# Optimization experiments

Measured on AMD Instinct MI355X. Metric: run time of the kernel, lower is better.

Reference implementation:

```python
import math
import jax, jax.numpy as jnp
import numpy as np

H = 16
D_MODEL = 1024
D_K = D_MODEL // H


def setup_inputs() -> dict:
    key = jax.random.key(0)
    ks = jax.random.split(key, 12)
    B, S = 4, 2048
    scale = 1.0 / math.sqrt(D_MODEL)
    inp = {
        "query": jax.random.normal(ks[0], (B, S, D_MODEL), jnp.float32),
        "key": jax.random.normal(ks[1], (B, S, D_MODEL), jnp.float32),
        "value": jax.random.normal(ks[2], (B, S, D_MODEL), jnp.float32),
        "mask": jnp.ones((B, 1, 1, S), jnp.int32),
        "Wq": jax.random.normal(ks[3], (D_MODEL, D_MODEL), jnp.float32) * scale,
        "bq": jnp.zeros((D_MODEL,), jnp.float32),
        "Wk": jax.random.normal(ks[4], (D_MODEL, D_MODEL), jnp.float32) * scale,
        "bk": jnp.zeros((D_MODEL,), jnp.float32),
        "Wv": jax.random.normal(ks[5], (D_MODEL, D_MODEL), jnp.float32) * scale,
        "bv": jnp.zeros((D_MODEL,), jnp.float32),
        "Wo": jax.random.normal(ks[6], (D_MODEL, D_MODEL), jnp.float32) * scale,
        "bo": jnp.zeros((D_MODEL,), jnp.float32),
    }
    return inp


def _split_heads(x, W, b):
    # x: (B, S, d_model) -> (B, H, S, d_k); torch Linear: x @ W.T + b
    B, S, _ = x.shape
    y = x @ W.T + b
    return y.reshape(B, S, H, D_K).transpose(0, 2, 1, 3)


def reference(query, key, value, mask, Wq, bq, Wk, bk, Wv, bv, Wo, bo):
    B, Sq, _ = query.shape
    q = _split_heads(query, Wq, bq)   # (B,H,Sq,dk)
    k = _split_heads(key, Wk, bk)     # (B,H,Skv,dk)
    v = _split_heads(value, Wv, bv)   # (B,H,Skv,dk)
    scores = jnp.einsum('bhqd,bhkd->bhqk', q, k) / math.sqrt(D_K)
    scores = jnp.where(mask == 0, jnp.float32(-1e9), scores)
    p_attn = jax.nn.softmax(scores, axis=-1)  # dropout p=0 (eval)
    x = jnp.einsum('bhqk,bhkd->bhqd', p_attn, v)
    x = x.transpose(0, 2, 1, 3).reshape(B, Sq, H * D_K)
    return x @ Wo.T + bo
```

## Files before the change

kernel.cpp:

```cpp
#include <hip/hip_runtime.h>
#include <hip/hip_bf16.h>
#include <stdint.h>

typedef unsigned short u16;
typedef short bf16x8 __attribute__((ext_vector_type(8)));
typedef float f32x4 __attribute__((ext_vector_type(4)));

#define D_MODEL 1024
#define NHEAD 16
#define DK 64
#define SEQ 2048
#define NB 4
#define MTOT (NB * SEQ)

__device__ __forceinline__ u16 f2bf(float f) {
  union { float f; unsigned u; } x; x.f = f;
  unsigned r = x.u + 0x7FFFu + ((x.u >> 16) & 1u);
  return (u16)(r >> 16);
}
#if __has_builtin(__builtin_amdgcn_cvt_pk_bf16_f32)
__device__ __forceinline__ unsigned pkbf(float a, float b) {
  auto r = __builtin_amdgcn_cvt_pk_bf16_f32(a, b);
  union { decltype(r) v; unsigned u; } c; c.v = r; return c.u;
}
#else
__device__ __forceinline__ unsigned pkbf(float a, float b) {
  return (unsigned)f2bf(a) | ((unsigned)f2bf(b) << 16);
}
#endif
__device__ __forceinline__ void gl_lds16(const u16* g, u16* s) {
  __builtin_amdgcn_global_load_lds(
      (const __attribute__((address_space(1))) void*)g,
      (__attribute__((address_space(3))) void*)s, 16, 0, 0);
}

__global__ __launch_bounds__(256) void cvt1(const float4* __restrict__ src,
                                            uint2* __restrict__ dst, int n4) {
  for (int i = blockIdx.x * 256 + threadIdx.x; i < n4; i += gridDim.x * 256) {
    float4 x = src[i];
    uint2 o;
    o.x = pkbf(x.x, x.y);
    o.y = pkbf(x.z, x.w);
    dst[i] = o;
  }
}
__global__ __launch_bounds__(256) void cvt4(const float4* __restrict__ s0,
                                            const float4* __restrict__ s1,
                                            const float4* __restrict__ s2,
                                            const float4* __restrict__ s3,
                                            uint2* __restrict__ dst, int n4each) {
  const float4* s = (blockIdx.y == 0) ? s0 : (blockIdx.y == 1) ? s1
                  : (blockIdx.y == 2) ? s2 : s3;
  uint2* d = dst + (size_t)blockIdx.y * n4each;
  for (int i = blockIdx.x * 256 + threadIdx.x; i < n4each; i += gridDim.x * 256) {
    float4 x = s[i];
    uint2 o;
    o.x = pkbf(x.x, x.y);
    o.y = pkbf(x.z, x.w);
    d[i] = o;
  }
}

template <int MODE>
__global__ __launch_bounds__(256) void gemm_bt128(
    const u16* __restrict__ A, const u16* __restrict__ W,
    const float* __restrict__ bias, void* __restrict__ out)
{
  __shared__ alignas(16) u16 smem[17408];
  u16* As = smem;
  u16* Bs = smem + 8192;

  const int tid = threadIdx.x;
  const int l = tid & 63, w = tid >> 6;
  const int wm = (w >> 1) << 6, wn = (w & 1) << 6;
  const int m0 = blockIdx.y << 7, n0 = blockIdx.x << 7;

  int srow[4], sk8[4], sdst[4];
#pragma unroll
  for (int r = 0; r < 4; ++r) {
    int c = r * 256 + tid;
    srow[r] = c >> 3;
    sk8[r] = (c & 7) ^ (srow[r] & 7);
    sdst[r] = c << 3;
  }
  int aoff[4][2], boff[4][2];
#pragma unroll
  for (int i = 0; i < 4; ++i) {
    int mr = wm + (i << 4) + (l & 15);
    int nr = wn + (i << 4) + (l & 15);
#pragma unroll
    for (int s = 0; s < 2; ++s) {
      int kc = (s << 2) + (l >> 4);
      aoff[i][s] = (mr << 6) + ((kc ^ (mr & 7)) << 3);
      boff[i][s] = (nr << 6) + ((kc ^ (nr & 7)) << 3);
    }
  }

  const u16* Ab = A + (size_t)m0 * D_MODEL;
  const u16* Bb = W + (size_t)n0 * D_MODEL;

  f32x4 acc[4][4] = {};

  for (int kt = 0; kt < 16; ++kt) {
    const int kbase = kt << 6;
#pragma unroll
    for (int r = 0; r < 4; ++r)
      gl_lds16(Ab + (size_t)srow[r] * D_MODEL + kbase + (sk8[r] << 3), As + sdst[r]);
#pragma unroll
    for (int r = 0; r < 4; ++r)
      gl_lds16(Bb + (size_t)srow[r] * D_MODEL + kbase + (sk8[r] << 3), Bs + sdst[r]);
    __syncthreads();
#pragma unroll
    for (int s = 0; s < 2; ++s) {
      bf16x8 af[4], bfv[4];
#pragma unroll
      for (int i = 0; i < 4; ++i) af[i] = *(const bf16x8*)(As + aoff[i][s]);
#pragma unroll
      for (int j = 0; j < 4; ++j) bfv[j] = *(const bf16x8*)(Bs + boff[j][s]);
#pragma unroll
      for (int i = 0; i < 4; ++i)
#pragma unroll
        for (int j = 0; j < 4; ++j)
          acc[i][j] = __builtin_amdgcn_mfma_f32_16x16x32_bf16(af[i], bfv[j], acc[i][j], 0, 0, 0);
    }
    __syncthreads();
  }

  if (MODE == 1) {
    u16* Cs = smem;
    u16* outb = (u16*)out;
#pragma unroll
    for (int i = 0; i < 4; ++i)
#pragma unroll
      for (int j = 0; j < 4; ++j) {
        int sl = wm + (i << 4) + ((l >> 4) << 2);
        int nl = wn + (j << 4) + (l & 15);
        float bj = bias[n0 + nl];
        uint2 pk;
        pk.x = pkbf(acc[i][j][0] + bj, acc[i][j][1] + bj);
        pk.y = pkbf(acc[i][j][2] + bj, acc[i][j][3] + bj);
        *(uint2*)(Cs + nl * 136 + sl) = pk;
      }
    __syncthreads();
    int nl = tid >> 1, sh = (tid & 1) << 6;
    int n = n0 + nl;
    int b_ = m0 >> 11;
    const uint4* src = (const uint4*)(Cs + nl * 136 + sh);
    uint4* dst = (uint4*)(outb +
        (((size_t)b_ * NHEAD + (n >> 6)) * DK + (n & 63)) * SEQ + (m0 & 2047) + sh);
#pragma unroll
    for (int e = 0; e < 8; ++e) dst[e] = src[e];
  } else {
    u16* outb = (u16*)out;
    float* outf = (float*)out;
#pragma unroll
    for (int i = 0; i < 4; ++i)
#pragma unroll
      for (int j = 0; j < 4; ++j) {
        int ml = m0 + wm + (i << 4) + ((l >> 4) << 2);
        int n = n0 + wn + (j << 4) + (l & 15);
        float bj = bias[n];
#pragma unroll
        for (int r = 0; r < 4; ++r) {
          int m = ml + r;
          float v = acc[i][j][r] + bj;
          if (MODE == 0)
            outb[(((size_t)(m >> 11) * NHEAD + (n >> 6)) * SEQ + (m & 2047)) * DK + (n & 63)] = f2bf(v);
          else
            outf[(size_t)m * D_MODEL + n] = v;
        }
      }
  }
}

__global__ __launch_bounds__(256, 4) void attn_fused(
    const u16* __restrict__ Q,
    const u16* __restrict__ K,
    const u16* __restrict__ Vt,
    const int* __restrict__ mask,
    u16* __restrict__ X)
{
  __shared__ alignas(16) u16 PQ[8192];
  __shared__ alignas(16) u16 Ks[4096];
  __shared__ alignas(16) u16 Vs[4096];
  __shared__ alignas(16) float mbf[64];

  const int tid = threadIdx.x;
  const int l = tid & 63, w = tid >> 6;
  const int lq = l & 15, qd = l >> 4;
  const int bh = blockIdx.y;
  const int q0 = blockIdx.x << 7;
  const int b_ = bh >> 4, h = bh & 15;
  const size_t base = (size_t)bh * SEQ * DK;
  const int wq0 = w << 5;

#pragma unroll
  for (int r = 0; r < 4; ++r) {
    int c = r * 256 + tid;
    int row = c >> 3, k8 = (c & 7) ^ (row & 7);
    gl_lds16(Q + base + (size_t)(q0 + row) * DK + (k8 << 3), PQ + (c << 3));
  }
  __syncthreads();

  bf16x8 qf[2][2];
#pragma unroll
  for (int i = 0; i < 2; ++i)
#pragma unroll
    for (int s = 0; s < 2; ++s) {
      int row = wq0 + (i << 4) + lq;
      int kc = (s << 2) + qd;
      qf[i][s] = *(const bf16x8*)(PQ + (row << 6) + ((kc ^ (row & 7)) << 3));
    }

  f32x4 Ov[2][4] = {};
  float lrow[2] = {0.f, 0.f};
  const float SC = 0.125f * 1.44269504088896f;

  for (int t = 0; t < 32; ++t) {
    const int kv0 = t << 6;
    __syncthreads();
#pragma unroll
    for (int r = 0; r < 2; ++r) {
      int c = r * 256 + tid;
      int row = c >> 3, k8 = (c & 7) ^ (row & 7);
      gl_lds16(K + base + (size_t)(kv0 + row) * DK + (k8 << 3), Ks + (c << 3));
    }
#pragma unroll
    for (int r = 0; r < 2; ++r) {
      int c = r * 256 + tid;
      int row = c >> 3, k8 = (c & 7) ^ (row & 7);
      gl_lds16(Vt + base + (size_t)row * SEQ + kv0 + (k8 << 3), Vs + (c << 3));
    }
    if (tid < 64)
      mbf[tid] = mask[b_ * SEQ + kv0 + tid] ? 0.0f : -1.44269504e9f;
    __syncthreads();

    f32x4 Sc[4][2] = {};
#pragma unroll
    for (int s = 0; s < 2; ++s) {
      bf16x8 kf[4];
#pragma unroll
      for (int jb = 0; jb < 4; ++jb) {
        int row = (jb << 4) + lq;
        int kc = (s << 2) + qd;
        kf[jb] = *(const bf16x8*)(Ks + (row << 6) + ((kc ^ (row & 7)) << 3));
      }
#pragma unroll
      for (int jb = 0; jb < 4; ++jb)
#pragma unroll
        for (int i = 0; i < 2; ++i)
          Sc[jb][i] = __builtin_amdgcn_mfma_f32_16x16x32_bf16(kf[jb], qf[i][s], Sc[jb][i], 0, 0, 0);
    }

    float4 m4[4];
#pragma unroll
    for (int jb = 0; jb < 4; ++jb) m4[jb] = *(const float4*)(mbf + (jb << 4) + (qd << 2));

#pragma unroll
    for (int i = 0; i < 2; ++i) {
      float sum = 0.f;
      const int prow = wq0 + (i << 4) + lq;
      const int rbase = prow << 6;
      const int rsw = prow & 7;
#pragma unroll
      for (int jb = 0; jb < 4; ++jb) {
        float p0 = exp2f(fmaf(Sc[jb][i][0], SC, m4[jb].x));
        float p1 = exp2f(fmaf(Sc[jb][i][1], SC, m4[jb].y));
        float p2 = exp2f(fmaf(Sc[jb][i][2], SC, m4[jb].z));
        float p3 = exp2f(fmaf(Sc[jb][i][3], SC, m4[jb].w));
        sum += (p0 + p1) + (p2 + p3);
        uint2 pk;
        pk.x = pkbf(p0, p1);
        pk.y = pkbf(p2, p3);
        int c = (jb << 1) + (qd >> 1);
        *(uint2*)(PQ + rbase + ((c ^ rsw) << 3) + ((qd & 1) << 2)) = pk;
      }
      sum += __shfl_xor(sum, 16);
      sum += __shfl_xor(sum, 32);
      lrow[i] += sum;
    }

#pragma unroll
    for (int s = 0; s < 2; ++s) {
      bf16x8 pf[2], vf[4];
#pragma unroll
      for (int i = 0; i < 2; ++i) {
        int prow = wq0 + (i << 4) + lq;
        pf[i] = *(const bf16x8*)(PQ + (prow << 6) + ((((s << 2) + qd) ^ (prow & 7)) << 3));
      }
#pragma unroll
      for (int j = 0; j < 4; ++j) {
        int row = (j << 4) + lq;
        int kc = (s << 2) + qd;
        vf[j] = *(const bf16x8*)(Vs + (row << 6) + ((kc ^ (row & 7)) << 3));
      }
#pragma unroll
      for (int i = 0; i < 2; ++i)
#pragma unroll
        for (int j = 0; j < 4; ++j)
          Ov[i][j] = __builtin_amdgcn_mfma_f32_16x16x32_bf16(pf[i], vf[j], Ov[i][j], 0, 0, 0);
    }
  }

#pragma unroll
  for (int i = 0; i < 2; ++i) {
    float li = 1.0f / lrow[i];
#pragma unroll
    for (int r = 0; r < 4; ++r) {
      float sc_ = __shfl(li, (l & 48) | ((qd << 2) + r));
      int qrow = q0 + wq0 + (i << 4) + (qd << 2) + r;
#pragma unroll
      for (int j = 0; j < 4; ++j)
        X[((size_t)b_ * SEQ + qrow) * D_MODEL + (h << 6) + (j << 4) + lq] =
            f2bf(Ov[i][j][r] * sc_);
    }
  }
}

extern "C" void kernel_launch(void* const* d_in, const int* in_sizes, int n_in,
                              void* d_out, int out_size, void* d_ws, size_t ws_size,
                              hipStream_t stream) {
  const float* query = (const float*)d_in[0];
  const float* key_  = (const float*)d_in[1];
  const float* value = (const float*)d_in[2];
  const int* mask    = (const int*)d_in[3];
  const float* Wq = (const float*)d_in[4];
  const float* bq = (const float*)d_in[5];
  const float* Wk = (const float*)d_in[6];
  const float* bk = (const float*)d_in[7];
  const float* Wv = (const float*)d_in[8];
  const float* bv = (const float*)d_in[9];
  const float* Wo = (const float*)d_in[10];
  const float* bo = (const float*)d_in[11];

  u16* ws16 = (u16*)d_ws;
  const size_t WSZ = (size_t)D_MODEL * D_MODEL;
  const size_t ASZ = (size_t)MTOT * D_MODEL;
  u16* wqc = ws16;
  u16* wkc = ws16 + WSZ;
  u16* wvc = ws16 + 2 * WSZ;
  u16* woc = ws16 + 3 * WSZ;
  u16* C1  = ws16 + 4 * WSZ;
  u16* Qb  = ws16 + 4 * WSZ + ASZ;
  u16* Kb  = ws16 + 4 * WSZ + 2 * ASZ;
  u16* Xb  = C1;
  u16* Vtb = (u16*)d_out;

  dim3 blk(256);
  dim3 gg(D_MODEL / 128, MTOT / 128);

  cvt4<<<dim3(256, 4), blk, 0, stream>>>((const float4*)Wq, (const float4*)Wk,
                                         (const float4*)Wv, (const float4*)Wo,
                                         (uint2*)wqc, (int)(WSZ / 4));
  cvt1<<<1024, blk, 0, stream>>>((const float4*)query, (uint2*)C1, (int)(ASZ / 4));
  gemm_bt128<0><<<gg, blk, 0, stream>>>(C1, wqc, bq, Qb);
  cvt1<<<1024, blk, 0, stream>>>((const float4*)key_, (uint2*)C1, (int)(ASZ / 4));
  gemm_bt128<0><<<gg, blk, 0, stream>>>(C1, wkc, bk, Kb);
  cvt1<<<1024, blk, 0, stream>>>((const float4*)value, (uint2*)C1, (int)(ASZ / 4));
  gemm_bt128<1><<<gg, blk, 0, stream>>>(C1, wvc, bv, Vtb);
  attn_fused<<<dim3(SEQ / 128, NB * NHEAD), blk, 0, stream>>>(Qb, Kb, Vtb, mask, Xb);
  gemm_bt128<2><<<gg, blk, 0, stream>>>(Xb, woc, bo, d_out);
}
```

Measured before the change: 407.8 us.

## Shrink GEMM tiles to 64x128, fold softmax scale into Q, compute row sums via MFMA

The projection GEMMs move from 128x128 to 64x128 tiles with a 4-blocks-per-CU launch bound, doubling the grid to improve occupancy and wave count. The softmax scale and log2e are folded into the Q projection epilogue, and the mask bias now initializes the score accumulator, so the exp step becomes a raw hardware exp2. Row sums are no longer reduced with shuffles: a ones row appended to the V tile makes an extra MFMA produce the denominators. Together these trim VALU and shuffle work in the attention loop, at the cost of lower per-block reuse in the GEMMs and one extra MFMA per step.

```diff
diff --git a/kernel.cpp b/kernel.cpp
--- a/kernel.cpp
+++ b/kernel.cpp
@@ -27,6 +27,11 @@
 __device__ __forceinline__ unsigned pkbf(float a, float b) {
   return (unsigned)f2bf(a) | ((unsigned)f2bf(b) << 16);
 }
+#endif
+#if __has_builtin(__builtin_amdgcn_exp2f)
+__device__ __forceinline__ float exp2r(float x) { return __builtin_amdgcn_exp2f(x); }
+#else
+__device__ __forceinline__ float exp2r(float x) { return exp2f(x); }
 #endif
 __device__ __forceinline__ void gl_lds16(const u16* g, u16* s) {
   __builtin_amdgcn_global_load_lds(
@@ -62,63 +67,70 @@
 }
 
 template <int MODE>
-__global__ __launch_bounds__(256) void gemm_bt128(
+__global__ __launch_bounds__(256, 4) void gemm_bt64(
     const u16* __restrict__ A, const u16* __restrict__ W,
-    const float* __restrict__ bias, void* __restrict__ out)
+    const float* __restrict__ bias, void* __restrict__ out, float scale)
 {
-  __shared__ alignas(16) u16 smem[17408];
+  __shared__ alignas(16) u16 smem[12288];
   u16* As = smem;
-  u16* Bs = smem + 8192;
+  u16* Bs = smem + 4096;
 
   const int tid = threadIdx.x;
   const int l = tid & 63, w = tid >> 6;
-  const int wm = (w >> 1) << 6, wn = (w & 1) << 6;
-  const int m0 = blockIdx.y << 7, n0 = blockIdx.x << 7;
-
-  int srow[4], sk8[4], sdst[4];
+  const int lq = l & 15, qd = l >> 4;
+  const int wm = (w >> 1) << 5, wn = (w & 1) << 6;
+  const int m0 = blockIdx.y << 6, n0 = blockIdx.x << 7;
+
+  int arow[2], ak8[2], brow[4], bk8[4];
+#pragma unroll
+  for (int r = 0; r < 2; ++r) {
+    int c = r * 256 + tid;
+    arow[r] = c >> 3; ak8[r] = (c & 7) ^ (arow[r] & 7);
+  }
 #pragma unroll
   for (int r = 0; r < 4; ++r) {
     int c = r * 256 + tid;
-    srow[r] = c >> 3;
-    sk8[r] = (c & 7) ^ (srow[r] & 7);
-    sdst[r] = c << 3;
-  }
-  int aoff[4][2], boff[4][2];
-#pragma unroll
-  for (int i = 0; i < 4; ++i) {
-    int mr = wm + (i << 4) + (l & 15);
-    int nr = wn + (i << 4) + (l & 15);
-#pragma unroll
-    for (int s = 0; s < 2; ++s) {
-      int kc = (s << 2) + (l >> 4);
-      aoff[i][s] = (mr << 6) + ((kc ^ (mr & 7)) << 3);
-      boff[i][s] = (nr << 6) + ((kc ^ (nr & 7)) << 3);
-    }
+    brow[r] = c >> 3; bk8[r] = (c & 7) ^ (brow[r] & 7);
+  }
+  int aoff[2][2], boff[4][2];
+#pragma unroll
+  for (int i = 0; i < 2; ++i) {
+    int mr = wm + (i << 4) + lq;
+#pragma unroll
+    for (int s = 0; s < 2; ++s)
+      aoff[i][s] = (mr << 6) + ((((s << 2) + qd) ^ (mr & 7)) << 3);
+  }
+#pragma unroll
+  for (int j = 0; j < 4; ++j) {
+    int nr = wn + (j << 4) + lq;
+#pragma unroll
+    for (int s = 0; s < 2; ++s)
+      boff[j][s] = (nr << 6) + ((((s << 2) + qd) ^ (nr & 7)) << 3);
   }
 
   const u16* Ab = A + (size_t)m0 * D_MODEL;
   const u16* Bb = W + (size_t)n0 * D_MODEL;
 
-  f32x4 acc[4][4] = {};
+  f32x4 acc[2][4] = {};
 
   for (int kt = 0; kt < 16; ++kt) {
     const int kbase = kt << 6;
 #pragma unroll
+    for (int r = 0; r < 2; ++r)
+      gl_lds16(Ab + (size_t)arow[r] * D_MODEL + kbase + (ak8[r] << 3), As + ((r * 256 + tid) << 3));
+#pragma unroll
     for (int r = 0; r < 4; ++r)
-      gl_lds16(Ab + (size_t)srow[r] * D_MODEL + kbase + (sk8[r] << 3), As + sdst[r]);
-#pragma unroll
-    for (int r = 0; r < 4; ++r)
-      gl_lds16(Bb + (size_t)srow[r] * D_MODEL + kbase + (sk8[r] << 3), Bs + sdst[r]);
+      gl_lds16(Bb + (size_t)brow[r] * D_MODEL + kbase + (bk8[r] << 3), Bs + ((r * 256 + tid) << 3));
     __syncthreads();
 #pragma unroll
     for (int s = 0; s < 2; ++s) {
-      bf16x8 af[4], bfv[4];
-#pragma unroll
-      for (int i = 0; i < 4; ++i) af[i] = *(const bf16x8*)(As + aoff[i][s]);
+      bf16x8 af[2], bfv[4];
+#pragma unroll
+      for (int i = 0; i < 2; ++i) af[i] = *(const bf16x8*)(As + aoff[i][s]);
 #pragma unroll
       for (int j = 0; j < 4; ++j) bfv[j] = *(const bf16x8*)(Bs + boff[j][s]);
 #pragma unroll
-      for (int i = 0; i < 4; ++i)
+      for (int i = 0; i < 2; ++i)
 #pragma unroll
         for (int j = 0; j < 4; ++j)
           acc[i][j] = __builtin_amdgcn_mfma_f32_16x16x32_bf16(af[i], bfv[j], acc[i][j], 0, 0, 0);
@@ -130,40 +142,40 @@
     u16* Cs = smem;
     u16* outb = (u16*)out;
 #pragma unroll
-    for (int i = 0; i < 4; ++i)
+    for (int i = 0; i < 2; ++i)
 #pragma unroll
       for (int j = 0; j < 4; ++j) {
-        int sl = wm + (i << 4) + ((l >> 4) << 2);
-        int nl = wn + (j << 4) + (l & 15);
+        int ml = wm + (i << 4) + (qd << 2);
+        int nl = wn + (j << 4) + lq;
         float bj = bias[n0 + nl];
         uint2 pk;
         pk.x = pkbf(acc[i][j][0] + bj, acc[i][j][1] + bj);
         pk.y = pkbf(acc[i][j][2] + bj, acc[i][j][3] + bj);
-        *(uint2*)(Cs + nl * 136 + sl) = pk;
-      }
-    __syncthreads();
-    int nl = tid >> 1, sh = (tid & 1) << 6;
+        *(uint2*)(Cs + nl * 80 + ml) = pk;
+      }
+    __syncthreads();
+    int nl = tid >> 1, sh = (tid & 1) << 5;
     int n = n0 + nl;
     int b_ = m0 >> 11;
-    const uint4* src = (const uint4*)(Cs + nl * 136 + sh);
+    const uint4* src = (const uint4*)(Cs + nl * 80 + sh);
     uint4* dst = (uint4*)(outb +
         (((size_t)b_ * NHEAD + (n >> 6)) * DK + (n & 63)) * SEQ + (m0 & 2047) + sh);
 #pragma unroll
-    for (int e = 0; e < 8; ++e) dst[e] = src[e];
+    for (int e = 0; e < 4; ++e) dst[e] = src[e];
   } else {
     u16* outb = (u16*)out;
     float* outf = (float*)out;
 #pragma unroll
-    for (int i = 0; i < 4; ++i)
+    for (int i = 0; i < 2; ++i)
 #pragma unroll
       for (int j = 0; j < 4; ++j) {
-        int ml = m0 + wm + (i << 4) + ((l >> 4) << 2);
-        int n = n0 + wn + (j << 4) + (l & 15);
+        int ml = m0 + wm + (i << 4) + (qd << 2);
+        int n = n0 + wn + (j << 4) + lq;
         float bj = bias[n];
 #pragma unroll
         for (int r = 0; r < 4; ++r) {
           int m = ml + r;
-          float v = acc[i][j][r] + bj;
+          float v = (acc[i][j][r] + bj) * scale;
           if (MODE == 0)
             outb[(((size_t)(m >> 11) * NHEAD + (n >> 6)) * SEQ + (m & 2047)) * DK + (n & 63)] = f2bf(v);
           else
@@ -182,7 +194,7 @@
 {
   __shared__ alignas(16) u16 PQ[8192];
   __shared__ alignas(16) u16 Ks[4096];
-  __shared__ alignas(16) u16 Vs[4096];
+  __shared__ alignas(16) u16 Vs[5120];
   __shared__ alignas(16) float mbf[64];
 
   const int tid = threadIdx.x;
@@ -200,6 +212,11 @@
     int row = c >> 3, k8 = (c & 7) ^ (row & 7);
     gl_lds16(Q + base + (size_t)(q0 + row) * DK + (k8 << 3), PQ + (c << 3));
   }
+  {
+    unsigned v = (tid < 16) ? 0x3F803F80u : 0u;
+    uint2 pk; pk.x = v; pk.y = v;
+    *(uint2*)(Vs + 4096 + tid * 4) = pk;
+  }
   __syncthreads();
 
   bf16x8 qf[2][2];
@@ -208,13 +225,11 @@
 #pragma unroll
     for (int s = 0; s < 2; ++s) {
       int row = wq0 + (i << 4) + lq;
-      int kc = (s << 2) + qd;
-      qf[i][s] = *(const bf16x8*)(PQ + (row << 6) + ((kc ^ (row & 7)) << 3));
+      qf[i][s] = *(const bf16x8*)(PQ + (row << 6) + ((((s << 2) + qd) ^ (row & 7)) << 3));
     }
 
   f32x4 Ov[2][4] = {};
-  float lrow[2] = {0.f, 0.f};
-  const float SC = 0.125f * 1.44269504088896f;
+  f32x4 Ovl[2] = {};
 
   for (int t = 0; t < 32; ++t) {
     const int kv0 = t << 6;
@@ -235,15 +250,25 @@
       mbf[tid] = mask[b_ * SEQ + kv0 + tid] ? 0.0f : -1.44269504e9f;
     __syncthreads();
 
-    f32x4 Sc[4][2] = {};
+    float4 m4[4];
+#pragma unroll
+    for (int jb = 0; jb < 4; ++jb) m4[jb] = *(const float4*)(mbf + (jb << 4) + (qd << 2));
+
+    f32x4 Sc[4][2];
+#pragma unroll
+    for (int jb = 0; jb < 4; ++jb)
+#pragma unroll
+      for (int i = 0; i < 2; ++i) {
+        Sc[jb][i][0] = m4[jb].x; Sc[jb][i][1] = m4[jb].y;
+        Sc[jb][i][2] = m4[jb].z; Sc[jb][i][3] = m4[jb].w;
+      }
 #pragma unroll
     for (int s = 0; s < 2; ++s) {
       bf16x8 kf[4];
 #pragma unroll
       for (int jb = 0; jb < 4; ++jb) {
         int row = (jb << 4) + lq;
-        int kc = (s << 2) + qd;
-        kf[jb] = *(const bf16x8*)(Ks + (row << 6) + ((kc ^ (row & 7)) << 3));
+        kf[jb] = *(const bf16x8*)(Ks + (row << 6) + ((((s << 2) + qd) ^ (row & 7)) << 3));
       }
 #pragma unroll
       for (int jb = 0; jb < 4; ++jb)
@@ -252,37 +277,28 @@
           Sc[jb][i] = __builtin_amdgcn_mfma_f32_16x16x32_bf16(kf[jb], qf[i][s], Sc[jb][i], 0, 0, 0);
     }
 
-    float4 m4[4];
-#pragma unroll
-    for (int jb = 0; jb < 4; ++jb) m4[jb] = *(const float4*)(mbf + (jb << 4) + (qd << 2));
-
 #pragma unroll
     for (int i = 0; i < 2; ++i) {
-      float sum = 0.f;
       const int prow = wq0 + (i << 4) + lq;
       const int rbase = prow << 6;
       const int rsw = prow & 7;
 #pragma unroll
       for (int jb = 0; jb < 4; ++jb) {
-        float p0 = exp2f(fmaf(Sc[jb][i][0], SC, m4[jb].x));
-        float p1 = exp2f(fmaf(Sc[jb][i][1], SC, m4[jb].y));
-        float p2 = exp2f(fmaf(Sc[jb][i][2], SC, m4[jb].z));
-        float p3 = exp2f(fmaf(Sc[jb][i][3], SC, m4[jb].w));
-        sum += (p0 + p1) + (p2 + p3);
+        float p0 = exp2r(Sc[jb][i][0]);
+        float p1 = exp2r(Sc[jb][i][1]);
+        float p2 = exp2r(Sc[jb][i][2]);
+        float p3 = exp2r(Sc[jb][i][3]);
         uint2 pk;
         pk.x = pkbf(p0, p1);
         pk.y = pkbf(p2, p3);
         int c = (jb << 1) + (qd >> 1);
         *(uint2*)(PQ + rbase + ((c ^ rsw) << 3) + ((qd & 1) << 2)) = pk;
       }
-      sum += __shfl_xor(sum, 16);
-      sum += __shfl_xor(sum, 32);
-      lrow[i] += sum;
     }
 
 #pragma unroll
     for (int s = 0; s < 2; ++s) {
-      bf16x8 pf[2], vf[4];
+      bf16x8 pf[2], vf[4], vf1;
 #pragma unroll
       for (int i = 0; i < 2; ++i) {
         int prow = wq0 + (i << 4) + lq;
@@ -291,23 +307,30 @@
 #pragma unroll
       for (int j = 0; j < 4; ++j) {
         int row = (j << 4) + lq;
-        int kc = (s << 2) + qd;
-        vf[j] = *(const bf16x8*)(Vs + (row << 6) + ((kc ^ (row & 7)) << 3));
-      }
-#pragma unroll
-      for (int i = 0; i < 2; ++i)
+        vf[j] = *(const bf16x8*)(Vs + (row << 6) + ((((s << 2) + qd) ^ (row & 7)) << 3));
+      }
+      {
+        int row = 64 + lq;
+        vf1 = *(const bf16x8*)(Vs + (row << 6) + ((((s << 2) + qd) ^ (row & 7)) << 3));
+      }
+#pragma unroll
+      for (int i = 0; i < 2; ++i) {
 #pragma unroll
         for (int j = 0; j < 4; ++j)
           Ov[i][j] = __builtin_amdgcn_mfma_f32_16x16x32_bf16(pf[i], vf[j], Ov[i][j], 0, 0, 0);
+        Ovl[i] = __builtin_amdgcn_mfma_f32_16x16x32_bf16(pf[i], vf1, Ovl[i], 0, 0, 0);
+      }
     }
   }
 
 #pragma unroll
   for (int i = 0; i < 2; ++i) {
-    float li = 1.0f / lrow[i];
+    float inv[4];
+#pragma unroll
+    for (int r = 0; r < 4; ++r) inv[r] = 1.0f / Ovl[i][r];
 #pragma unroll
     for (int r = 0; r < 4; ++r) {
-      float sc_ = __shfl(li, (l & 48) | ((qd << 2) + r));
+      float sc_ = __shfl(inv[r], l & 48);
       int qrow = q0 + wq0 + (i << 4) + (qd << 2) + r;
 #pragma unroll
       for (int j = 0; j < 4; ++j)
@@ -346,18 +369,20 @@
   u16* Xb  = C1;
   u16* Vtb = (u16*)d_out;
 
+  const float SCQ = 0.125f * 1.44269504088896f;
+
   dim3 blk(256);
-  dim3 gg(D_MODEL / 128, MTOT / 128);
+  dim3 gg(D_MODEL / 128, MTOT / 64);
 
   cvt4<<<dim3(256, 4), blk, 0, stream>>>((const float4*)Wq, (const float4*)Wk,
                                          (const float4*)Wv, (const float4*)Wo,
                                          (uint2*)wqc, (int)(WSZ / 4));
   cvt1<<<1024, blk, 0, stream>>>((const float4*)query, (uint2*)C1, (int)(ASZ / 4));
-  gemm_bt128<0><<<gg, blk, 0, stream>>>(C1, wqc, bq, Qb);
+  gemm_bt64<0><<<gg, blk, 0, stream>>>(C1, wqc, bq, Qb, SCQ);
   cvt1<<<1024, blk, 0, stream>>>((const float4*)key_, (uint2*)C1, (int)(ASZ / 4));
-  gemm_bt128<0><<<gg, blk, 0, stream>>>(C1, wkc, bk, Kb);
+  gemm_bt64<0><<<gg, blk, 0, stream>>>(C1, wkc, bk, Kb, 1.0f);
   cvt1<<<1024, blk, 0, stream>>>((const float4*)value, (uint2*)C1, (int)(ASZ / 4));
-  gemm_bt128<1><<<gg, blk, 0, stream>>>(C1, wvc, bv, Vtb);
+  gemm_bt64<1><<<gg, blk, 0, stream>>>(C1, wvc, bv, Vtb, 1.0f);
   attn_fused<<<dim3(SEQ / 128, NB * NHEAD), blk, 0, stream>>>(Qb, Kb, Vtb, mask, Xb);
-  gemm_bt128<2><<<gg, blk, 0, stream>>>(Xb, woc, bo, d_out);
-}
+  gemm_bt64<2><<<gg, blk, 0, stream>>>(Xb, woc, bo, d_out, 1.0f);
+}
```

Result: faster. 363.7 us (-10.8%).
